# Kernel optimization log

Measured on AMD Instinct MI355X. Metric: run time of the kernel, lower is better.

The kernel has to match this reference:

```python
import jax, jax.numpy as jnp
import numpy as np

B, N_SPEC = 4096, 1024
N_R1, N_R2 = 2048, 8192


def setup_inputs() -> dict:
    key = jax.random.key(0)
    ks = jax.random.split(key, 8)
    t_in = jax.random.uniform(ks[0], (B,), dtype=jnp.float32, minval=0.1, maxval=1.0)
    y_in = jax.random.uniform(ks[1], (B, N_SPEC), dtype=jnp.float32)
    k1 = jax.random.uniform(ks[2], (N_R1,), dtype=jnp.float32)
    k2 = jax.random.uniform(ks[3], (N_R2,), dtype=jnp.float32)
    inds_1r = jax.random.randint(ks[4], (N_R1,), 0, N_SPEC, dtype=jnp.int32)
    inds_1p = jax.random.randint(ks[5], (N_R1,), 0, N_SPEC, dtype=jnp.int32)
    inds_2r = jax.random.randint(ks[6], (N_R2, 2), 0, N_SPEC, dtype=jnp.int32)
    inds_2p = jax.random.randint(ks[7], (N_R2,), 0, N_SPEC, dtype=jnp.int32)
    return dict(t_in=t_in, y_in=y_in, k1=k1, k2=k2,
                inds_1r=inds_1r, inds_1p=inds_1p, inds_2r=inds_2r, inds_2p=inds_2p)


def reference(t_in, y_in, k1, k2, inds_1r, inds_1p, inds_2r, inds_2p):
    # rate_i(t): time-dependent rates, shape [B, n_react]
    rate_1 = t_in[:, None] * k1[None, :]          # [B, N_R1]
    rate_2 = t_in[:, None] * k2[None, :]          # [B, N_R2]

    # 1st-order: gather reactant concentrations, multiply by rates, scatter into products
    term_1 = y_in[:, inds_1r] * rate_1            # [B, N_R1]
    # 2nd-order: product of the two reactant concentrations times rate
    term_2 = y_in[:, inds_2r].prod(axis=-1) * rate_2  # [B, N_R2]

    y_out = jnp.zeros_like(y_in)
    y_out = y_out.at[:, inds_1p].add(term_1)
    y_out = y_out.at[:, inds_2p].add(term_2)
    return y_out
```

## Files before the change

### kernel.cpp

```cpp
#include <hip/hip_runtime.h>
#include <hip/hip_fp16.h>


constexpr int BATCH = 4096;
constexpr int NS    = 1024;
constexpr int NR1   = 2048;
constexpr int NR2   = 8192;
constexpr int NRT   = NR1 + NR2;
constexpr int G     = 8;
constexpr int MAIN_THREADS = 512;
constexpr int NHALF = 2 * NS;
constexpr int MAX_HSLOTS = 32;

constexpr int POISON = (int)0xAAAAAAAAu;

constexpr size_t WS_CURSOR = 0;
constexpr size_t WS_ELL    = 8192;

union H2x4 {
    float4  f4;
    __half2 h2[4];
};

__global__ __launch_bounds__(256) void fill_kernel(
    const float* __restrict__ k1,  const float* __restrict__ k2,
    const int*   __restrict__ i1r, const int*   __restrict__ i1p,
    const int*   __restrict__ i2r, const int*   __restrict__ i2p,
    int*         __restrict__ cursor,
    int2*        __restrict__ ell)
{
    const int i = blockIdx.x * blockDim.x + threadIdx.x;
    int p, packed; float kf;
    if (i < NR1) {
        p = i1p[i];
        packed = i1r[i] | (NS << 16);
        kf = k1[i];
    } else if (i < NRT) {
        const int r = i - NR1;
        p = i2p[r];
        packed = i2r[2 * r] | (i2r[2 * r + 1] << 16);
        kf = k2[r];
    } else return;
    const unsigned kh = (unsigned)__half_as_ushort(__float2half(kf));
    const int kbits = (int)(kh | (kh << 16));
    const int slot = atomicAdd(&cursor[p], 1) - POISON;
    const int row = slot >> 1;
    if (row < MAX_HSLOTS)
        ell[row * NHALF + 2 * p + (slot & 1)] = make_int2(packed, kbits);
}

__device__ __forceinline__ void apply_rec(int pack, int kbits, bool valid,
                                          const float4* __restrict__ y_h,
                                          __half2 acc[4])
{
    const unsigned ix = (unsigned)pack;
    H2x4 ya, yb;
    ya.f4 = y_h[ix & 0xFFFFu];
    yb.f4 = y_h[ix >> 16];
    int kb = valid ? kbits : 0;
    const __half2 kk = *reinterpret_cast<const __half2*>(&kb);
    #pragma unroll
    for (int j = 0; j < 4; ++j)
        acc[j] = __hfma2(kk, __hmul2(ya.h2[j], yb.h2[j]), acc[j]);
}

__global__ __launch_bounds__(MAIN_THREADS) void reaction_main_kernel(
    const float* __restrict__ t_in,
    const float* __restrict__ y_in,
    const int*   __restrict__ cursor,
    const int4*  __restrict__ ell4,
    float*       __restrict__ y_out)
{
    __shared__ float4 y_h[NS + 1];

    const int tid = threadIdx.x;
    const int b0  = blockIdx.x * G;
    const float* __restrict__ yb0 = y_in + (size_t)b0 * NS;

    #pragma unroll
    for (int h = 0; h < 2; ++h) {
        const int s = tid + 512 * h;
        H2x4 v;
        v.h2[0] = __halves2half2(__float2half(yb0[0 * NS + s]), __float2half(yb0[1 * NS + s]));
        v.h2[1] = __halves2half2(__float2half(yb0[2 * NS + s]), __float2half(yb0[3 * NS + s]));
        v.h2[2] = __halves2half2(__float2half(yb0[4 * NS + s]), __float2half(yb0[5 * NS + s]));
        v.h2[3] = __halves2half2(__float2half(yb0[6 * NS + s]), __float2half(yb0[7 * NS + s]));
        y_h[s] = v.f4;
    }
    if (tid == 0) {
        H2x4 one;
        const __half2 o = __float2half2_rn(1.0f);
        one.h2[0] = o; one.h2[1] = o; one.h2[2] = o; one.h2[3] = o;
        y_h[NS] = one.f4;
    }
    __syncthreads();

    const int2 craw = ((const int2*)cursor)[tid];
    const int c0 = craw.x - POISON;
    const int c1 = craw.y - POISON;
    const int cmax = min((max(c0, c1) + 1) >> 1, MAX_HSLOTS);

    __half2 accA[4], accB[4];
    #pragma unroll
    for (int j = 0; j < 4; ++j) {
        accA[j] = __float2half2_rn(0.0f);
        accB[j] = __float2half2_rn(0.0f);
    }

    const int col0 = 2 * tid;
    int4 ra = ell4[col0];
    int4 rb = ell4[col0 + 1];

    for (int slot = 0; slot < cmax; ++slot) {
        const int4 na = ell4[(slot + 1) * NS + col0];
        const int4 nb = ell4[(slot + 1) * NS + col0 + 1];
        const int s2 = 2 * slot;
        apply_rec(ra.x, ra.y, s2     < c0, y_h, accA);
        apply_rec(ra.z, ra.w, s2 + 1 < c0, y_h, accA);
        apply_rec(rb.x, rb.y, s2     < c1, y_h, accB);
        apply_rec(rb.z, rb.w, s2 + 1 < c1, y_h, accB);
        ra = na; rb = nb;
    }

    float t[G];
    #pragma unroll
    for (int r = 0; r < G; ++r) t[r] = t_in[b0 + r];

    float* __restrict__ ob0 = y_out + (size_t)b0 * NS;
    const int p0 = 2 * tid;
    #pragma unroll
    for (int j = 0; j < 4; ++j) {
        const float2 fA = __half22float2(accA[j]);
        const float2 fB = __half22float2(accB[j]);
        *(float2*)(ob0 + (size_t)(2 * j)     * NS + p0) =
            make_float2(fA.x * t[2 * j],     fB.x * t[2 * j]);
        *(float2*)(ob0 + (size_t)(2 * j + 1) * NS + p0) =
            make_float2(fA.y * t[2 * j + 1], fB.y * t[2 * j + 1]);
    }
}

extern "C" void kernel_launch(void* const* d_in, const int* in_sizes, int n_in,
                              void* d_out, int out_size, void* d_ws, size_t ws_size,
                              hipStream_t stream) {
    const float* t_in = (const float*)d_in[0];
    const float* y_in = (const float*)d_in[1];
    const float* k1   = (const float*)d_in[2];
    const float* k2   = (const float*)d_in[3];
    const int*   i1r  = (const int*)d_in[4];
    const int*   i1p  = (const int*)d_in[5];
    const int*   i2r  = (const int*)d_in[6];
    const int*   i2p  = (const int*)d_in[7];
    float*       out  = (float*)d_out;

    char* ws = (char*)d_ws;
    int*  cursor = (int*)(ws + WS_CURSOR);
    int2* ell    = (int2*)(ws + WS_ELL);

    fill_kernel<<<dim3((NRT + 255) / 256), dim3(256), 0, stream>>>(
        k1, k2, i1r, i1p, i2r, i2p, cursor, ell);
    reaction_main_kernel<<<dim3(BATCH / G), dim3(MAIN_THREADS), 0, stream>>>(
        t_in, y_in, cursor, (const int4*)ell, out);
}
```

Measured before the change: 96.03 us.

## Split output products across two blocks, one product per thread

The main kernel now runs a 2D grid where blockIdx.y picks half of the 1024 products, so each thread accumulates one product column instead of two. This halves per-thread accumulator and load state and doubles the block count, and the launch bounds now request 8 blocks per SM for higher occupancy. The cost is that each block still converts and stages all 1024 species of its batch group into shared memory, so the y_in read and half-conversion work is done twice. Output stores become scalar instead of float2.

```diff
diff --git a/kernel.cpp b/kernel.cpp
--- a/kernel.cpp
+++ b/kernel.cpp
@@ -64,7 +64,7 @@
         acc[j] = __hfma2(kk, __hmul2(ya.h2[j], yb.h2[j]), acc[j]);
 }
 
-__global__ __launch_bounds__(MAIN_THREADS) void reaction_main_kernel(
+__global__ __launch_bounds__(MAIN_THREADS, 8) void reaction_main_kernel(
     const float* __restrict__ t_in,
     const float* __restrict__ y_in,
     const int*   __restrict__ cursor,
@@ -95,47 +95,29 @@
     }
     __syncthreads();
 
-    const int2 craw = ((const int2*)cursor)[tid];
-    const int c0 = craw.x - POISON;
-    const int c1 = craw.y - POISON;
-    const int cmax = min((max(c0, c1) + 1) >> 1, MAX_HSLOTS);
+    const int p = (blockIdx.y << 9) | tid;
+    const int c = cursor[p] - POISON;
+    const int cmax = min((c + 1) >> 1, MAX_HSLOTS);
 
-    __half2 accA[4], accB[4];
+    __half2 acc[4];
+    #pragma unroll
+    for (int j = 0; j < 4; ++j) acc[j] = __float2half2_rn(0.0f);
+
+    int4 ra = ell4[p];
+    for (int slot = 0; slot < cmax; ++slot) {
+        const int4 na = ell4[(slot + 1) * NS + p];
+        const int s2 = 2 * slot;
+        apply_rec(ra.x, ra.y, s2     < c, y_h, acc);
+        apply_rec(ra.z, ra.w, s2 + 1 < c, y_h, acc);
+        ra = na;
+    }
+
+    float* __restrict__ ob0 = y_out + (size_t)b0 * NS;
     #pragma unroll
     for (int j = 0; j < 4; ++j) {
-        accA[j] = __float2half2_rn(0.0f);
-        accB[j] = __float2half2_rn(0.0f);
-    }
-
-    const int col0 = 2 * tid;
-    int4 ra = ell4[col0];
-    int4 rb = ell4[col0 + 1];
-
-    for (int slot = 0; slot < cmax; ++slot) {
-        const int4 na = ell4[(slot + 1) * NS + col0];
-        const int4 nb = ell4[(slot + 1) * NS + col0 + 1];
-        const int s2 = 2 * slot;
-        apply_rec(ra.x, ra.y, s2     < c0, y_h, accA);
-        apply_rec(ra.z, ra.w, s2 + 1 < c0, y_h, accA);
-        apply_rec(rb.x, rb.y, s2     < c1, y_h, accB);
-        apply_rec(rb.z, rb.w, s2 + 1 < c1, y_h, accB);
-        ra = na; rb = nb;
-    }
-
-    float t[G];
-    #pragma unroll
-    for (int r = 0; r < G; ++r) t[r] = t_in[b0 + r];
-
-    float* __restrict__ ob0 = y_out + (size_t)b0 * NS;
-    const int p0 = 2 * tid;
-    #pragma unroll
-    for (int j = 0; j < 4; ++j) {
-        const float2 fA = __half22float2(accA[j]);
-        const float2 fB = __half22float2(accB[j]);
-        *(float2*)(ob0 + (size_t)(2 * j)     * NS + p0) =
-            make_float2(fA.x * t[2 * j],     fB.x * t[2 * j]);
-        *(float2*)(ob0 + (size_t)(2 * j + 1) * NS + p0) =
-            make_float2(fA.y * t[2 * j + 1], fB.y * t[2 * j + 1]);
+        const float2 f = __half22float2(acc[j]);
+        ob0[(size_t)(2 * j)     * NS + p] = f.x * t_in[b0 + 2 * j];
+        ob0[(size_t)(2 * j + 1) * NS + p] = f.y * t_in[b0 + 2 * j + 1];
     }
 }
 
@@ -158,6 +140,6 @@
 
     fill_kernel<<<dim3((NRT + 255) / 256), dim3(256), 0, stream>>>(
         k1, k2, i1r, i1p, i2r, i2p, cursor, ell);
-    reaction_main_kernel<<<dim3(BATCH / G), dim3(MAIN_THREADS), 0, stream>>>(
+    reaction_main_kernel<<<dim3(BATCH / G, 2), dim3(MAIN_THREADS), 0, stream>>>(
         t_in, y_in, cursor, (const int4*)ell, out);
 }
```

Result: no change. 95.25 us (-0.8%).

## Fuse ELL build and reaction compute into one cooperative kernel with grid sync

Applied to the files above, without the earlier changes.

Merges the fill kernel that builds the per-product ELL reaction table into the main compute kernel. The first blocks' threads do the atomic slot assignment and release-store the records, then a cooperative grid-wide sync precedes the table reads. This removes the second kernel launch and its inter-kernel gap. In exchange it adds a grid barrier across 512 blocks of 512 threads, which must all be co-resident (launch bounds raised to 4 blocks per CU), and the barrier serializes the y staging in shared memory behind the slowest block.

```diff
diff --git a/kernel.cpp b/kernel.cpp
--- a/kernel.cpp
+++ b/kernel.cpp
@@ -1,5 +1,8 @@
 #include <hip/hip_runtime.h>
 #include <hip/hip_fp16.h>
+#include <hip/hip_cooperative_groups.h>
+
+namespace cg = cooperative_groups;
 
 
 constexpr int BATCH = 4096;
@@ -22,33 +25,6 @@
     __half2 h2[4];
 };
 
-__global__ __launch_bounds__(256) void fill_kernel(
-    const float* __restrict__ k1,  const float* __restrict__ k2,
-    const int*   __restrict__ i1r, const int*   __restrict__ i1p,
-    const int*   __restrict__ i2r, const int*   __restrict__ i2p,
-    int*         __restrict__ cursor,
-    int2*        __restrict__ ell)
-{
-    const int i = blockIdx.x * blockDim.x + threadIdx.x;
-    int p, packed; float kf;
-    if (i < NR1) {
-        p = i1p[i];
-        packed = i1r[i] | (NS << 16);
-        kf = k1[i];
-    } else if (i < NRT) {
-        const int r = i - NR1;
-        p = i2p[r];
-        packed = i2r[2 * r] | (i2r[2 * r + 1] << 16);
-        kf = k2[r];
-    } else return;
-    const unsigned kh = (unsigned)__half_as_ushort(__float2half(kf));
-    const int kbits = (int)(kh | (kh << 16));
-    const int slot = atomicAdd(&cursor[p], 1) - POISON;
-    const int row = slot >> 1;
-    if (row < MAX_HSLOTS)
-        ell[row * NHALF + 2 * p + (slot & 1)] = make_int2(packed, kbits);
-}
-
 __device__ __forceinline__ void apply_rec(int pack, int kbits, bool valid,
                                           const float4* __restrict__ y_h,
                                           __half2 acc[4])
@@ -64,10 +40,14 @@
         acc[j] = __hfma2(kk, __hmul2(ya.h2[j], yb.h2[j]), acc[j]);
 }
 
-__global__ __launch_bounds__(MAIN_THREADS) void reaction_main_kernel(
+__global__ __launch_bounds__(MAIN_THREADS, 4) void reaction_fused_kernel(
     const float* __restrict__ t_in,
     const float* __restrict__ y_in,
-    const int*   __restrict__ cursor,
+    const float* __restrict__ k1,  const float* __restrict__ k2,
+    const int*   __restrict__ i1r, const int* __restrict__ i1p,
+    const int*   __restrict__ i2r, const int* __restrict__ i2p,
+    int*         __restrict__ cursor,
+    long long*   __restrict__ ell_ll,
     const int4*  __restrict__ ell4,
     float*       __restrict__ y_out)
 {
@@ -76,6 +56,32 @@
     const int tid = threadIdx.x;
     const int b0  = blockIdx.x * G;
     const float* __restrict__ yb0 = y_in + (size_t)b0 * NS;
+
+    const int gi = blockIdx.x * MAIN_THREADS + tid;
+    if (gi < NRT) {
+        int p, packed; float kf;
+        if (gi < NR1) {
+            p = i1p[gi];
+            packed = i1r[gi] | (NS << 16);
+            kf = k1[gi];
+        } else {
+            const int r = gi - NR1;
+            p = i2p[r];
+            packed = i2r[2 * r] | (i2r[2 * r + 1] << 16);
+            kf = k2[r];
+        }
+        const unsigned kh = (unsigned)__half_as_ushort(__float2half(kf));
+        const int kbits = (int)(kh | (kh << 16));
+        const int slot = atomicAdd(&cursor[p], 1) - POISON;
+        const int row  = slot >> 1;
+        if (row < MAX_HSLOTS) {
+            const long long rec =
+                (long long)(unsigned)packed | ((long long)kbits << 32);
+            __hip_atomic_store(
+                &ell_ll[(size_t)row * NHALF + 2 * p + (slot & 1)], rec,
+                __ATOMIC_RELEASE, __HIP_MEMORY_SCOPE_AGENT);
+        }
+    }
 
     #pragma unroll
     for (int h = 0; h < 2; ++h) {
@@ -93,7 +99,8 @@
         one.h2[0] = o; one.h2[1] = o; one.h2[2] = o; one.h2[3] = o;
         y_h[NS] = one.f4;
     }
-    __syncthreads();
+
+    cg::this_grid().sync();
 
     const int2 craw = ((const int2*)cursor)[tid];
     const int c0 = craw.x - POISON;
@@ -152,12 +159,17 @@
     const int*   i2p  = (const int*)d_in[7];
     float*       out  = (float*)d_out;
 
-    char* ws = (char*)d_ws;
-    int*  cursor = (int*)(ws + WS_CURSOR);
-    int2* ell    = (int2*)(ws + WS_ELL);
+    char*       ws     = (char*)d_ws;
+    int*        cursor = (int*)(ws + WS_CURSOR);
+    long long*  ell_ll = (long long*)(ws + WS_ELL);
+    const int4* ell4   = (const int4*)(ws + WS_ELL);
 
-    fill_kernel<<<dim3((NRT + 255) / 256), dim3(256), 0, stream>>>(
-        k1, k2, i1r, i1p, i2r, i2p, cursor, ell);
-    reaction_main_kernel<<<dim3(BATCH / G), dim3(MAIN_THREADS), 0, stream>>>(
-        t_in, y_in, cursor, (const int4*)ell, out);
+    void* args[] = {
+        (void*)&t_in, (void*)&y_in, (void*)&k1, (void*)&k2,
+        (void*)&i1r,  (void*)&i1p,  (void*)&i2r, (void*)&i2p,
+        (void*)&cursor, (void*)&ell_ll, (void*)&ell4, (void*)&out
+    };
+    hipLaunchCooperativeKernel((const void*)reaction_fused_kernel,
+                               dim3(BATCH / G), dim3(MAIN_THREADS),
+                               args, 0, stream);
 }
```

Result: slower. 171.5 us (+78.6%).
